# Kernel optimization log

Measured on AMD Instinct MI355X. Metric: run time of the kernel, lower is better.

The kernel has to match this reference:

```python
import jax, jax.numpy as jnp
import numpy as np

B, L, D, H = 4, 256, 256, 8
DH = D // H


def setup_inputs() -> dict:
    key = jax.random.key(0)
    ks = jax.random.split(key, 12)
    s = 1.0 / np.sqrt(D)
    return {
        "inputs": jax.random.normal(ks[0], (B, L, D), jnp.float32),
        "mask": jax.random.bernoulli(ks[1], 0.15, (B, L, L)),
        "rel_emb": jax.random.normal(ks[2], (B, L, L, D), jnp.float32) * 0.05,
        "Wq": jax.random.normal(ks[3], (D, D), jnp.float32) * s,
        "bq": jnp.zeros((D,), jnp.float32),
        "Wk": jax.random.normal(ks[4], (D, D), jnp.float32) * s,
        "bk": jnp.zeros((D,), jnp.float32),
        "Wv": jax.random.normal(ks[5], (D, D), jnp.float32) * s,
        "bv": jnp.zeros((D,), jnp.float32),
        "Wo": jax.random.normal(ks[6], (D, D), jnp.float32) * s,
        "bo": jnp.zeros((D,), jnp.float32),
        "u": jax.random.normal(ks[7], (D,), jnp.float32),
        "v_param": jax.random.normal(ks[8], (D,), jnp.float32),
    }


def _shape(x):
    # (B, L, D) -> (B, H, L, DH)
    return x.reshape(B, L, H, DH).transpose(0, 2, 1, 3)


def reference(inputs, mask, rel_emb, Wq, bq, Wk, bk, Wv, bv, Wo, bo, u, v_param):
    q = _shape(inputs @ Wq.T + bq) / np.sqrt(DH)  # (B,H,L,DH), pre-scaled
    k = _shape(inputs @ Wk.T + bk)
    val = _shape(inputs @ Wv.T + bv)

    u_h = u.reshape(1, H, 1, DH)
    v_h = v_param.reshape(1, H, 1, DH)

    # content term: (q+u) k^T
    a_c = jnp.einsum('bhqd,bhkd->bhqk', q + u_h, k)
    # position term: (q+v) rel_emb^T, rel_emb per (q,k) pair
    rel = rel_emb.reshape(B, L, L, H, DH)
    b_d = jnp.einsum('bhqd,bqkhd->bhqk', q + v_h, rel)

    scores = (a_c + b_d).astype(jnp.float32)
    scores = jnp.where(mask[:, None, :, :], -1e18, scores)
    attn = jax.nn.softmax(scores, axis=-1)  # (B,H,L,L)

    ctx = jnp.einsum('bhqk,bhkd->bhqd', attn, val)
    ctx = ctx.transpose(0, 2, 1, 3).reshape(B, L, D)
    out = ctx @ Wo.T + bo
    return (out, attn)
```

## Files before the change

kernel.cpp:

```cpp
#include <hip/hip_runtime.h>
#include <hip/hip_bf16.h>

#define BB  4
#define LL  256
#define DD  256
#define HH  8
#define DHH 32
#define BL  1024

__global__ __launch_bounds__(256) void qkv_kernel(
    const float* __restrict__ X,
    const float* __restrict__ Wq, const float* __restrict__ bq,
    const float* __restrict__ Wk, const float* __restrict__ bk,
    const float* __restrict__ Wv, const float* __restrict__ bv,
    const float* __restrict__ u,  const float* __restrict__ vp,
    const unsigned int* __restrict__ mask_w,
    float* __restrict__ qu, float* __restrict__ qv,
    float* __restrict__ K,  float* __restrict__ V,
    unsigned int* __restrict__ flags) {
  const int t = threadIdx.x;
  if (blockIdx.x == 256) {
    __shared__ int sf32, shib;
    if (t == 0) { sf32 = 0; shib = 0; }
    __syncthreads();
    int f = 0, hb = 0;
    for (int i = t; i < 16384; i += 256) {
      unsigned int x = mask_w[i];
      if (x == 0x3F800000u) f = 1;
      else if (x & 0xFFFFFF00u) hb = 1;
    }
    if (f)  atomicOr(&sf32, 1);
    if (hb) atomicOr(&shib, 1);
    __syncthreads();
    if (t == 0) flags[0] = (sf32 || !shib) ? 1u : 0u;
    return;
  }
  const int row0 = blockIdx.x * 4;
  const int c = t;
  float accq[4] = {0.f, 0.f, 0.f, 0.f};
  float acck[4] = {0.f, 0.f, 0.f, 0.f};
  float accv[4] = {0.f, 0.f, 0.f, 0.f};
  const float4* Wq4 = (const float4*)(Wq + c * DD);
  const float4* Wk4 = (const float4*)(Wk + c * DD);
  const float4* Wv4 = (const float4*)(Wv + c * DD);
  const float4* X4  = (const float4*)X;
  const int xbase = row0 * (DD / 4);
#pragma unroll 8
  for (int j4 = 0; j4 < DD / 4; ++j4) {
    const float4 wq = Wq4[j4], wk = Wk4[j4], wv = Wv4[j4];
#pragma unroll
    for (int r = 0; r < 4; ++r) {
      const float4 x = X4[xbase + r * (DD / 4) + j4];
      accq[r] += x.x * wq.x + x.y * wq.y + x.z * wq.z + x.w * wq.w;
      acck[r] += x.x * wk.x + x.y * wk.y + x.z * wk.z + x.w * wk.w;
      accv[r] += x.x * wv.x + x.y * wv.y + x.z * wv.z + x.w * wv.w;
    }
  }
  const float scale = 0.17677669529663687f;
  const float uc = u[c], vc = vp[c], bqc = bq[c], bkc = bk[c], bvc = bv[c];
#pragma unroll
  for (int r = 0; r < 4; ++r) {
    const int idx = (row0 + r) * DD + c;
    const float pq = (accq[r] + bqc) * scale;
    qu[idx] = pq + uc;
    qv[idx] = pq + vc;
    K[idx]  = acck[r] + bkc;
    V[idx]  = accv[r] + bvc;
  }
}

__global__ __launch_bounds__(512, 4) void attn_kernel(
    const float* __restrict__ qu, const float* __restrict__ qv,
    const float* __restrict__ Km, const float* __restrict__ Vm,
    const float* __restrict__ rel, const void* __restrict__ mask_raw,
    const unsigned int* __restrict__ flags,
    float* __restrict__ attn_out, float* __restrict__ ctx) {
  const int blk = blockIdx.x;
  const int xcd = blk & 7;
  const int b = xcd >> 1;
  const int q0 = ((xcd & 1) * 64 + (blk >> 3)) * 2;
  const int t = threadIdx.x;
  const int wave = t >> 6, lane = t & 63;
  __shared__ float qu_s[2][DD], qv_s[2][DD];
  __shared__ float msk_s[2][LL];
  __shared__ float sc[2][HH][LL + 4];
  __shared__ float pctx[2][HH][DD + 4];

  {
    const int qq = t >> 8, d = t & 255;
    const int bq = b * LL + q0 + qq;
    qu_s[qq][d] = qu[bq * DD + d];
    qv_s[qq][d] = qv[bq * DD + d];
    bool masked;
    if (flags[0]) masked = ((const unsigned int*)mask_raw)[bq * LL + d] != 0u;
    else          masked = ((const unsigned char*)mask_raw)[bq * LL + d] != 0;
    msk_s[qq][d] = masked ? 1.f : 0.f;
  }
  __syncthreads();

  const float4 u40 = ((const float4*)qu_s[0])[lane];
  const float4 u41 = ((const float4*)qu_s[1])[lane];
  const float4 w40 = ((const float4*)qv_s[0])[lane];
  const float4 w41 = ((const float4*)qv_s[1])[lane];
  const int hol = lane >> 3;
  const int k0 = wave * 32;
  const float4* K4  = (const float4*)(Km + (size_t)b * LL * DD) +
                      (size_t)k0 * 64 + lane;
  const float4* R40 = (const float4*)rel +
                      (size_t)(b * LL + q0) * (LL * 64) + (size_t)k0 * 64 + lane;
  const float4* R41 = R40 + (size_t)LL * 64;
#pragma unroll 4
  for (int i = 0; i < 32; ++i) {
    const int k = k0 + i;
    const float4 kk = K4[(size_t)i * 64];
    const float4 r0 = R40[(size_t)i * 64];
    const float4 r1 = R41[(size_t)i * 64];
    float s0 = u40.x * kk.x + u40.y * kk.y + u40.z * kk.z + u40.w * kk.w
             + w40.x * r0.x + w40.y * r0.y + w40.z * r0.z + w40.w * r0.w;
    float s1 = u41.x * kk.x + u41.y * kk.y + u41.z * kk.z + u41.w * kk.w
             + w41.x * r1.x + w41.y * r1.y + w41.z * r1.z + w41.w * r1.w;
    s0 += __shfl_xor(s0, 1); s0 += __shfl_xor(s0, 2); s0 += __shfl_xor(s0, 4);
    s1 += __shfl_xor(s1, 1); s1 += __shfl_xor(s1, 2); s1 += __shfl_xor(s1, 4);
    if ((lane & 7) == 0) {
      sc[0][hol][k] = (msk_s[0][k] != 0.f) ? -1e18f : s0;
      sc[1][hol][k] = (msk_s[1][k] != 0.f) ? -1e18f : s1;
    }
  }
  __syncthreads();

#pragma unroll
  for (int pp = 0; pp < 2; ++pp) {
    const int pair = wave + pp * 8;
    const int qq = pair >> 3, h = pair & 7;
    float v0 = sc[qq][h][lane], v1 = sc[qq][h][lane + 64];
    float v2 = sc[qq][h][lane + 128], v3 = sc[qq][h][lane + 192];
    float m = fmaxf(fmaxf(v0, v1), fmaxf(v2, v3));
#pragma unroll
    for (int off = 32; off >= 1; off >>= 1) m = fmaxf(m, __shfl_xor(m, off));
    float e0 = __expf(v0 - m), e1 = __expf(v1 - m);
    float e2 = __expf(v2 - m), e3 = __expf(v3 - m);
    float s = (e0 + e1) + (e2 + e3);
#pragma unroll
    for (int off = 32; off >= 1; off >>= 1) s += __shfl_xor(s, off);
    const float inv = 1.0f / s;
    e0 *= inv; e1 *= inv; e2 *= inv; e3 *= inv;
    sc[qq][h][lane] = e0; sc[qq][h][lane + 64] = e1;
    sc[qq][h][lane + 128] = e2; sc[qq][h][lane + 192] = e3;
    float* aout = attn_out + (((size_t)(b * HH + h) * LL + (q0 + qq)) * LL);
    aout[lane] = e0; aout[lane + 64] = e1;
    aout[lane + 128] = e2; aout[lane + 192] = e3;
  }
  __syncthreads();

  {
    const float4* V4 = (const float4*)(Vm + (size_t)b * LL * DD) +
                       (size_t)k0 * 64 + lane;
    float4 a0 = make_float4(0.f, 0.f, 0.f, 0.f);
    float4 a1 = make_float4(0.f, 0.f, 0.f, 0.f);
#pragma unroll 4
    for (int i = 0; i < 32; ++i) {
      const int k = k0 + i;
      const float p0 = sc[0][hol][k];
      const float p1 = sc[1][hol][k];
      const float4 vv = V4[(size_t)i * 64];
      a0.x += p0 * vv.x; a0.y += p0 * vv.y; a0.z += p0 * vv.z; a0.w += p0 * vv.w;
      a1.x += p1 * vv.x; a1.y += p1 * vv.y; a1.z += p1 * vv.z; a1.w += p1 * vv.w;
    }
    ((float4*)&pctx[0][wave][0])[lane] = a0;
    ((float4*)&pctx[1][wave][0])[lane] = a1;
  }
  __syncthreads();

  {
    const int qq = t >> 8, d = t & 255;
    float s = 0.f;
#pragma unroll
    for (int w = 0; w < HH; ++w) s += pctx[qq][w][d];
    ctx[(size_t)(b * LL + q0 + qq) * DD + d] = s;
  }
}

__global__ __launch_bounds__(256) void outproj_kernel(
    const float* __restrict__ ctx, const float* __restrict__ Wo,
    const float* __restrict__ bo, float* __restrict__ out) {
  const int row0 = blockIdx.x * 4;
  const int c = threadIdx.x;
  float acc[4] = {0.f, 0.f, 0.f, 0.f};
  const float4* W4 = (const float4*)(Wo + c * DD);
  const float4* X4 = (const float4*)ctx;
  const int xbase = row0 * (DD / 4);
#pragma unroll 8
  for (int j4 = 0; j4 < DD / 4; ++j4) {
    const float4 w = W4[j4];
#pragma unroll
    for (int r = 0; r < 4; ++r) {
      const float4 x = X4[xbase + r * (DD / 4) + j4];
      acc[r] += x.x * w.x + x.y * w.y + x.z * w.z + x.w * w.w;
    }
  }
  const float boc = bo[c];
#pragma unroll
  for (int r = 0; r < 4; ++r) out[(row0 + r) * DD + c] = acc[r] + boc;
}

extern "C" void kernel_launch(void* const* d_in, const int* in_sizes, int n_in,
                              void* d_out, int out_size, void* d_ws, size_t ws_size,
                              hipStream_t stream) {
  (void)in_sizes; (void)n_in; (void)out_size; (void)ws_size;
  const float* X   = (const float*)d_in[0];
  const void*  msk = d_in[1];
  const float* rel = (const float*)d_in[2];
  const float* Wq  = (const float*)d_in[3];
  const float* bq  = (const float*)d_in[4];
  const float* Wk  = (const float*)d_in[5];
  const float* bk  = (const float*)d_in[6];
  const float* Wv  = (const float*)d_in[7];
  const float* bv  = (const float*)d_in[8];
  const float* Wo  = (const float*)d_in[9];
  const float* bo  = (const float*)d_in[10];
  const float* u   = (const float*)d_in[11];
  const float* vp  = (const float*)d_in[12];

  float* out  = (float*)d_out;
  float* attn = out + BL * DD;

  float* ws_f = (float*)d_ws;
  float* qu  = ws_f;
  float* qv  = qu + BL * DD;
  float* K   = qv + BL * DD;
  float* V   = K  + BL * DD;
  float* ctx = V  + BL * DD;
  unsigned int* flags = (unsigned int*)(ctx + BL * DD);

  qkv_kernel<<<257, 256, 0, stream>>>(X, Wq, bq, Wk, bk, Wv, bv, u, vp,
                                      (const unsigned int*)msk,
                                      qu, qv, K, V, flags);
  attn_kernel<<<BL / 2, 512, 0, stream>>>(qu, qv, K, V, rel, msk, flags,
                                          attn, ctx);
  outproj_kernel<<<BL / 4, 256, 0, stream>>>(ctx, Wo, bo, out);
}
```

Baseline: 99.59 us.

## Split rel_emb position-term into separate streaming kernel, batch 4 queries per attention block

Moves the b_d position term, which streams the 256 MB rel_emb tensor, into its own kernel with 4096 small blocks to raise memory-level parallelism. The attention kernel now handles 4 queries per block, reusing each K/V load across more queries, and reads the precomputed b_d from a workspace buffer. This adds an extra kernel launch and a round trip of the b_d scores through global memory, and the larger shared-memory footprint lowers occupancy of the attention kernel.

```diff
diff --git a/kernel.cpp b/kernel.cpp
--- a/kernel.cpp
+++ b/kernel.cpp
@@ -69,71 +69,109 @@
   }
 }
 
-__global__ __launch_bounds__(512, 4) void attn_kernel(
-    const float* __restrict__ qu, const float* __restrict__ qv,
-    const float* __restrict__ Km, const float* __restrict__ Vm,
-    const float* __restrict__ rel, const void* __restrict__ mask_raw,
-    const unsigned int* __restrict__ flags,
+__global__ __launch_bounds__(256) void bd_kernel(
+    const float* __restrict__ qv, const float* __restrict__ rel,
+    float* __restrict__ bd) {
+  const int blk = blockIdx.x;
+  const int bq = blk >> 2, kc = blk & 3;
+  const int t = threadIdx.x, wave = t >> 6, lane = t & 63;
+  __shared__ float qv_s[DD];
+  __shared__ float sc[HH][68];
+  qv_s[t] = qv[bq * DD + t];
+  __syncthreads();
+  const float4 w4 = ((const float4*)qv_s)[lane];
+  const int hol = lane >> 3;
+  const int kr0 = wave * 16;
+  const float4* R4 = (const float4*)rel +
+                     ((size_t)bq * LL + kc * 64 + kr0) * 64 + lane;
+#pragma unroll 8
+  for (int i = 0; i < 16; ++i) {
+    const float4 rr = R4[(size_t)i * 64];
+    float s = w4.x * rr.x + w4.y * rr.y + w4.z * rr.z + w4.w * rr.w;
+    s += __shfl_xor(s, 1);
+    s += __shfl_xor(s, 2);
+    s += __shfl_xor(s, 4);
+    if ((lane & 7) == 0) sc[hol][kr0 + i] = s;
+  }
+  __syncthreads();
+  int idx = t;
+#pragma unroll
+  for (int r = 0; r < 2; ++r, idx += 256) {
+    const int h = idx >> 6, kr = idx & 63;
+    bd[((size_t)bq * HH + h) * LL + kc * 64 + kr] = sc[h][kr];
+  }
+}
+
+__global__ __launch_bounds__(512) void attn2_kernel(
+    const float* __restrict__ qu, const float* __restrict__ Km,
+    const float* __restrict__ Vm, const float* __restrict__ bd,
+    const void* __restrict__ mask_raw, const unsigned int* __restrict__ flags,
     float* __restrict__ attn_out, float* __restrict__ ctx) {
   const int blk = blockIdx.x;
   const int xcd = blk & 7;
   const int b = xcd >> 1;
-  const int q0 = ((xcd & 1) * 64 + (blk >> 3)) * 2;
-  const int t = threadIdx.x;
-  const int wave = t >> 6, lane = t & 63;
-  __shared__ float qu_s[2][DD], qv_s[2][DD];
-  __shared__ float msk_s[2][LL];
-  __shared__ float sc[2][HH][LL + 4];
-  __shared__ float pctx[2][HH][DD + 4];
-
+  const int q0 = ((xcd & 1) * 32 + (blk >> 3)) * 4;
+  const int t = threadIdx.x, wave = t >> 6, lane = t & 63;
+  __shared__ float qu_s[4][DD];
+  __shared__ float msk_s[4][LL];
+  __shared__ float sc[4][HH][264];
+  __shared__ float pctx[4][HH][264];
+
+  for (int idx = t; idx < 4 * DD; idx += 512) {
+    const int qq = idx >> 8, d = idx & 255;
+    qu_s[qq][d] = qu[(size_t)(b * LL + q0 + qq) * DD + d];
+  }
   {
-    const int qq = t >> 8, d = t & 255;
-    const int bq = b * LL + q0 + qq;
-    qu_s[qq][d] = qu[bq * DD + d];
-    qv_s[qq][d] = qv[bq * DD + d];
-    bool masked;
-    if (flags[0]) masked = ((const unsigned int*)mask_raw)[bq * LL + d] != 0u;
-    else          masked = ((const unsigned char*)mask_raw)[bq * LL + d] != 0;
-    msk_s[qq][d] = masked ? 1.f : 0.f;
-  }
-  __syncthreads();
-
-  const float4 u40 = ((const float4*)qu_s[0])[lane];
-  const float4 u41 = ((const float4*)qu_s[1])[lane];
-  const float4 w40 = ((const float4*)qv_s[0])[lane];
-  const float4 w41 = ((const float4*)qv_s[1])[lane];
+    const int use32 = flags[0];
+    for (int idx = t; idx < 4 * LL; idx += 512) {
+      const int qq = idx >> 8, k = idx & 255;
+      const size_t mi = (size_t)(b * LL + q0 + qq) * LL + k;
+      bool masked;
+      if (use32) masked = ((const unsigned int*)mask_raw)[mi] != 0u;
+      else       masked = ((const unsigned char*)mask_raw)[mi] != 0;
+      msk_s[qq][k] = masked ? 1.f : 0.f;
+    }
+  }
+  __syncthreads();
+
   const int hol = lane >> 3;
   const int k0 = wave * 32;
-  const float4* K4  = (const float4*)(Km + (size_t)b * LL * DD) +
-                      (size_t)k0 * 64 + lane;
-  const float4* R40 = (const float4*)rel +
-                      (size_t)(b * LL + q0) * (LL * 64) + (size_t)k0 * 64 + lane;
-  const float4* R41 = R40 + (size_t)LL * 64;
-#pragma unroll 4
+  float4 u4q[4];
+#pragma unroll
+  for (int qq = 0; qq < 4; ++qq) u4q[qq] = ((const float4*)qu_s[qq])[lane];
+  const float4* K4 = (const float4*)(Km + (size_t)b * LL * DD) +
+                     (size_t)k0 * 64 + lane;
+#pragma unroll 2
   for (int i = 0; i < 32; ++i) {
     const int k = k0 + i;
     const float4 kk = K4[(size_t)i * 64];
-    const float4 r0 = R40[(size_t)i * 64];
-    const float4 r1 = R41[(size_t)i * 64];
-    float s0 = u40.x * kk.x + u40.y * kk.y + u40.z * kk.z + u40.w * kk.w
-             + w40.x * r0.x + w40.y * r0.y + w40.z * r0.z + w40.w * r0.w;
-    float s1 = u41.x * kk.x + u41.y * kk.y + u41.z * kk.z + u41.w * kk.w
-             + w41.x * r1.x + w41.y * r1.y + w41.z * r1.z + w41.w * r1.w;
+    float s0 = u4q[0].x*kk.x + u4q[0].y*kk.y + u4q[0].z*kk.z + u4q[0].w*kk.w;
+    float s1 = u4q[1].x*kk.x + u4q[1].y*kk.y + u4q[1].z*kk.z + u4q[1].w*kk.w;
+    float s2 = u4q[2].x*kk.x + u4q[2].y*kk.y + u4q[2].z*kk.z + u4q[2].w*kk.w;
+    float s3 = u4q[3].x*kk.x + u4q[3].y*kk.y + u4q[3].z*kk.z + u4q[3].w*kk.w;
     s0 += __shfl_xor(s0, 1); s0 += __shfl_xor(s0, 2); s0 += __shfl_xor(s0, 4);
     s1 += __shfl_xor(s1, 1); s1 += __shfl_xor(s1, 2); s1 += __shfl_xor(s1, 4);
+    s2 += __shfl_xor(s2, 1); s2 += __shfl_xor(s2, 2); s2 += __shfl_xor(s2, 4);
+    s3 += __shfl_xor(s3, 1); s3 += __shfl_xor(s3, 2); s3 += __shfl_xor(s3, 4);
     if ((lane & 7) == 0) {
-      sc[0][hol][k] = (msk_s[0][k] != 0.f) ? -1e18f : s0;
-      sc[1][hol][k] = (msk_s[1][k] != 0.f) ? -1e18f : s1;
-    }
-  }
-  __syncthreads();
-
-#pragma unroll
-  for (int pp = 0; pp < 2; ++pp) {
-    const int pair = wave + pp * 8;
+      sc[0][hol][k] = s0; sc[1][hol][k] = s1;
+      sc[2][hol][k] = s2; sc[3][hol][k] = s3;
+    }
+  }
+  __syncthreads();
+
+#pragma unroll
+  for (int pp = 0; pp < 4; ++pp) {
+    const int pair = wave * 4 + pp;
     const int qq = pair >> 3, h = pair & 7;
-    float v0 = sc[qq][h][lane], v1 = sc[qq][h][lane + 64];
-    float v2 = sc[qq][h][lane + 128], v3 = sc[qq][h][lane + 192];
+    const float4 bb =
+        ((const float4*)(bd + ((size_t)(b * LL + q0 + qq) * HH + h) * LL))[lane];
+    const float4 ss = *(const float4*)&sc[qq][h][lane * 4];
+    const float4 mm = ((const float4*)msk_s[qq])[lane];
+    float v0 = (mm.x != 0.f) ? -1e18f : ss.x + bb.x;
+    float v1 = (mm.y != 0.f) ? -1e18f : ss.y + bb.y;
+    float v2 = (mm.z != 0.f) ? -1e18f : ss.z + bb.z;
+    float v3 = (mm.w != 0.f) ? -1e18f : ss.w + bb.w;
     float m = fmaxf(fmaxf(v0, v1), fmaxf(v2, v3));
 #pragma unroll
     for (int off = 32; off >= 1; off >>= 1) m = fmaxf(m, __shfl_xor(m, off));
@@ -144,35 +182,36 @@
     for (int off = 32; off >= 1; off >>= 1) s += __shfl_xor(s, off);
     const float inv = 1.0f / s;
     e0 *= inv; e1 *= inv; e2 *= inv; e3 *= inv;
-    sc[qq][h][lane] = e0; sc[qq][h][lane + 64] = e1;
-    sc[qq][h][lane + 128] = e2; sc[qq][h][lane + 192] = e3;
+    *(float4*)&sc[qq][h][lane * 4] = make_float4(e0, e1, e2, e3);
     float* aout = attn_out + (((size_t)(b * HH + h) * LL + (q0 + qq)) * LL);
-    aout[lane] = e0; aout[lane + 64] = e1;
-    aout[lane + 128] = e2; aout[lane + 192] = e3;
+    ((float4*)aout)[lane] = make_float4(e0, e1, e2, e3);
   }
   __syncthreads();
 
   {
     const float4* V4 = (const float4*)(Vm + (size_t)b * LL * DD) +
                        (size_t)k0 * 64 + lane;
-    float4 a0 = make_float4(0.f, 0.f, 0.f, 0.f);
-    float4 a1 = make_float4(0.f, 0.f, 0.f, 0.f);
-#pragma unroll 4
+    float4 a0 = make_float4(0.f,0.f,0.f,0.f), a1 = a0, a2 = a0, a3 = a0;
+#pragma unroll 2
     for (int i = 0; i < 32; ++i) {
       const int k = k0 + i;
-      const float p0 = sc[0][hol][k];
-      const float p1 = sc[1][hol][k];
       const float4 vv = V4[(size_t)i * 64];
-      a0.x += p0 * vv.x; a0.y += p0 * vv.y; a0.z += p0 * vv.z; a0.w += p0 * vv.w;
-      a1.x += p1 * vv.x; a1.y += p1 * vv.y; a1.z += p1 * vv.z; a1.w += p1 * vv.w;
-    }
-    ((float4*)&pctx[0][wave][0])[lane] = a0;
-    ((float4*)&pctx[1][wave][0])[lane] = a1;
-  }
-  __syncthreads();
-
-  {
-    const int qq = t >> 8, d = t & 255;
+      const float p0 = sc[0][hol][k], p1 = sc[1][hol][k];
+      const float p2 = sc[2][hol][k], p3 = sc[3][hol][k];
+      a0.x += p0*vv.x; a0.y += p0*vv.y; a0.z += p0*vv.z; a0.w += p0*vv.w;
+      a1.x += p1*vv.x; a1.y += p1*vv.y; a1.z += p1*vv.z; a1.w += p1*vv.w;
+      a2.x += p2*vv.x; a2.y += p2*vv.y; a2.z += p2*vv.z; a2.w += p2*vv.w;
+      a3.x += p3*vv.x; a3.y += p3*vv.y; a3.z += p3*vv.z; a3.w += p3*vv.w;
+    }
+    *(float4*)&pctx[0][wave][lane * 4] = a0;
+    *(float4*)&pctx[1][wave][lane * 4] = a1;
+    *(float4*)&pctx[2][wave][lane * 4] = a2;
+    *(float4*)&pctx[3][wave][lane * 4] = a3;
+  }
+  __syncthreads();
+
+  for (int idx = t; idx < 4 * DD; idx += 512) {
+    const int qq = idx >> 8, d = idx & 255;
     float s = 0.f;
 #pragma unroll
     for (int w = 0; w < HH; ++w) s += pctx[qq][w][d];
@@ -231,11 +270,12 @@
   float* V   = K  + BL * DD;
   float* ctx = V  + BL * DD;
   unsigned int* flags = (unsigned int*)(ctx + BL * DD);
+  float* bd  = (float*)(flags + 16);
 
   qkv_kernel<<<257, 256, 0, stream>>>(X, Wq, bq, Wk, bk, Wv, bv, u, vp,
                                       (const unsigned int*)msk,
                                       qu, qv, K, V, flags);
-  attn_kernel<<<BL / 2, 512, 0, stream>>>(qu, qv, K, V, rel, msk, flags,
-                                          attn, ctx);
+  bd_kernel<<<4096, 256, 0, stream>>>(qv, rel, bd);
+  attn2_kernel<<<256, 512, 0, stream>>>(qu, K, V, bd, msk, flags, attn, ctx);
   outproj_kernel<<<BL / 4, 256, 0, stream>>>(ctx, Wo, bo, out);
 }
```

Result: slower. 113.5 us (+13.9%).
